# Optimization experiments

Measured on AMD Instinct MI355X. Metric: run time of the kernel, lower is better.

Reference implementation:

```python
import jax, jax.numpy as jnp
import numpy as np

EPS = 1e-5

def _conv(x, w, b):
    # NCHW x OIHW -> NCHW, stride 1, SAME padding (stencil center (1,1) of 3x3, or 1x1)
    y = jax.lax.conv_general_dilated(x, w, (1, 1), 'SAME',
                                     dimension_numbers=('NCHW', 'OIHW', 'NCHW'))
    return y + b[None, :, None, None]

def _bn(x, gamma, beta):
    # training-mode batchnorm: stats over (N, H, W) per channel
    mean = jnp.mean(x, axis=(0, 2, 3), keepdims=True)
    var = jnp.var(x, axis=(0, 2, 3), keepdims=True)
    xhat = (x - mean) * jax.lax.rsqrt(var + EPS)
    return xhat * gamma[None, :, None, None] + beta[None, :, None, None]

def setup_inputs() -> dict:
    key = jax.random.key(0)
    ks = jax.random.split(key, 12)
    B, Cin, Cout, H, W = 2, 64, 64, 512, 512
    s = 0.05
    return {
        'x':  jax.random.normal(ks[0], (B, Cin, H, W), jnp.float32),
        'w1': jax.random.normal(ks[1], (Cout, Cin, 3, 3), jnp.float32) * s,
        'b1': jnp.zeros((Cout,), jnp.float32),
        'g1': jnp.ones((Cout,), jnp.float32),
        'be1': jnp.zeros((Cout,), jnp.float32),
        'w2': jax.random.normal(ks[2], (Cout, Cout, 3, 3), jnp.float32) * s,
        'b2': jnp.zeros((Cout,), jnp.float32),
        'g2': jnp.ones((Cout,), jnp.float32),
        'be2': jnp.zeros((Cout,), jnp.float32),
        'wp': jax.random.normal(ks[3], (Cout, Cin, 1, 1), jnp.float32) * s,
        'bp': jnp.zeros((Cout,), jnp.float32),
        'gp': jnp.ones((Cout,), jnp.float32),
        'bep': jnp.zeros((Cout,), jnp.float32),
    }

def reference(x, w1, b1, g1, be1, w2, b2, g2, be2, wp, bp, gp, bep):
    # project branch: 1x1 conv ([(0,0)] stencil) + BN
    residual = _bn(_conv(x, wp, bp), gp, bep)
    # conv1: pad + 3x3 lattice conv (full cp stencil) + BN + Identity downsample + ReLU
    out = jax.nn.relu(_bn(_conv(x, w1, b1), g1, be1))
    # conv2: pad + 3x3 lattice conv + BN
    out = _bn(_conv(out, w2, b2), g2, be2)
    # residual add + output ReLU
    return jax.nn.relu(out + residual)
```

## Files before the change

kernel.cpp:

```cpp
#include <hip/hip_runtime.h>
#include <hip/hip_bf16.h>
#include <stdint.h>

typedef short short8 __attribute__((ext_vector_type(8)));
typedef float f32x4 __attribute__((ext_vector_type(4)));
typedef float f32x16 __attribute__((ext_vector_type(16)));
typedef unsigned int u32;
typedef unsigned short u16;

#define HH 512
#define WW 512
#define CC 64
#define PLANE (HH*WW)
#define NSTATF 524288.0f

#define KTW 32
#define HSTR 560
#define KBSTR 1120
#define SLOTB 4480
#define NSLOT 8
#define RINGB (NSLOT*SLOTB)
#define BOUNCEB 8192
#define NBC 1024
#define NBP 4096
#define K5S 260

__device__ __forceinline__ u16 f2bf(float f) {
  __hip_bfloat16 h = __float2bfloat16(f);
  return __builtin_bit_cast(u16, h);
}
__device__ __forceinline__ u32 pk2bf(float a, float b) {
  return (u32)f2bf(a) | ((u32)f2bf(b) << 16);
}
__device__ __forceinline__ float bf2f(u16 u) {
  u32 x = ((u32)u) << 16;
  return __builtin_bit_cast(float, x);
}
__device__ __forceinline__ void lds_barrier() {
  asm volatile("s_waitcnt lgkmcnt(0)" ::: "memory");
  __builtin_amdgcn_s_barrier();
  __builtin_amdgcn_sched_barrier(0);
}

__global__ __launch_bounds__(512) void kprep(const float* __restrict__ w1,
    const float* __restrict__ w2, const float* __restrict__ wp,
    u16* __restrict__ wb1, u16* __restrict__ wb2, u16* __restrict__ wbp)
{
  const int id = blockIdx.x*512 + threadIdx.x;
  const int lane = id & 63;
  if (id < 9216) {
    const float* w = (id < 4608) ? w1 : w2;
    u16* o = (id < 4608) ? wb1 : wb2;
    const int fid = (id < 4608) ? (id >> 6) : ((id - 4608) >> 6);
    const int ct4 = fid / 18, rem = fid % 18;
    const int tap = rem >> 1, kb = rem & 1;
    const int cout = ct4*16 + (lane & 15);
    const int k0c = kb*32 + (lane >> 4)*8;
    u32 ow[4];
#pragma unroll
    for (int p = 0; p < 4; ++p) {
      float a = w[(size_t)(cout*64 + k0c + p*2    )*9 + tap];
      float b = w[(size_t)(cout*64 + k0c + p*2 + 1)*9 + tap];
      ow[p] = pk2bf(a, b);
    }
    *(uint4*)(o + ((size_t)fid*64 + lane)*8) = make_uint4(ow[0],ow[1],ow[2],ow[3]);
  } else if (id < 9728) {
    const int fid = (id - 9216) >> 6;
    const int ct = fid >> 2, kb = fid & 3;
    const int cout = ct*32 + (lane & 31);
    const int cinb = kb*16 + (lane >> 5)*8;
    u32 ow[4];
#pragma unroll
    for (int p = 0; p < 4; ++p)
      ow[p] = pk2bf(wp[cout*64 + cinb + p*2], wp[cout*64 + cinb + p*2 + 1]);
    *(uint4*)(wbp + ((size_t)fid*64 + lane)*8) = make_uint4(ow[0],ow[1],ow[2],ow[3]);
  }
}

__global__ __launch_bounds__(256) void k0(const float* __restrict__ x,
    const u16* __restrict__ wbp,
    u16* __restrict__ xh, u16* __restrict__ yp,
    float* __restrict__ psp, float* __restrict__ pqp)
{
  __shared__ __align__(16) u32 Tp[32*260];
  __shared__ __align__(16) char B2[32768];
  const int tid = threadIdx.x;
  const int lane = tid & 63, wv = tid >> 6;
  const int ct = wv & 1, tg = wv >> 1;
  const int wt = blockIdx.x, h = blockIdx.y, n = blockIdx.z;
  const int w0 = wt*256;
  const int bid0 = (n*HH + h)*2 + wt;

  short8 wpf[4];
#pragma unroll
  for (int kb = 0; kb < 4; ++kb)
    wpf[kb] = *(const short8*)(wbp + ((size_t)(ct*4 + kb)*64 + lane)*8);

  const float* xp = x + (size_t)n*CC*PLANE + (size_t)h*WW + w0;
#pragma unroll
  for (int it = 0; it < 8; ++it) {
    const int j = it*256 + tid;
    const int c2 = j >> 6, w4 = (j & 63) << 2;
    const f32x4 a = *(const f32x4*)(xp + (size_t)(c2*2    )*PLANE + w4);
    const f32x4 b = *(const f32x4*)(xp + (size_t)(c2*2 + 1)*PLANE + w4);
    uint4 o;
    o.x = pk2bf(a[0], b[0]);
    o.y = pk2bf(a[1], b[1]);
    o.z = pk2bf(a[2], b[2]);
    o.w = pk2bf(a[3], b[3]);
    *(uint4*)(Tp + (u32)c2*260 + w4) = o;
  }
  __syncthreads();
  u16* op = xh + ((size_t)(n*HH + h)*WW + w0)*CC;
#pragma unroll
  for (int it = 0; it < 8; ++it) {
    const int j = it*256 + tid;
    const int w = j >> 3, c8 = j & 7;
    uint4 o;
    o.x = Tp[(u32)(c8*4 + 0)*260 + w];
    o.y = Tp[(u32)(c8*4 + 1)*260 + w];
    o.z = Tp[(u32)(c8*4 + 2)*260 + w];
    o.w = Tp[(u32)(c8*4 + 3)*260 + w];
    *(uint4*)(op + (size_t)w*CC + c8*8) = o;
    *(uint4*)(B2 + (((u32)(w*128 + c8*16)) ^ (((u32)(w & 7)) << 4))) = o;
  }
  __syncthreads();
  f32x16 pa[4];
  float s[16], q[16];
#pragma unroll
  for (int r = 0; r < 16; ++r) { s[r] = 0.f; q[r] = 0.f; }
#pragma unroll
  for (int ti = 0; ti < 4; ++ti) {
    const int tl = tg + ti*2;
    const int pos = tl*32 + (lane & 31);
    f32x16 acc;
#pragma unroll
    for (int r = 0; r < 16; ++r) acc[r] = 0.f;
#pragma unroll
    for (int kb = 0; kb < 4; ++kb) {
      const short8 bf = *(const short8*)(B2 +
          (((u32)(pos*128 + kb*32 + (lane>>5)*16)) ^ (((u32)(pos & 7)) << 4)));
      acc = __builtin_amdgcn_mfma_f32_32x32x16_bf16(wpf[kb], bf, acc, 0, 0, 0);
    }
#pragma unroll
    for (int r = 0; r < 16; ++r) {
      const float v = acc[r];
      pa[ti][r] = v; s[r] += v; q[r] = fmaf(v, v, q[r]);
    }
  }
  __syncthreads();
#pragma unroll
  for (int ti = 0; ti < 4; ++ti) {
    const int tl = tg + ti*2;
    const int pos = tl*32 + (lane & 31);
    const int rp[8] = {0,2,8,10,16,18,24,26};
#pragma unroll
    for (int p = 0; p < 8; ++p) {
      const int co = ct*32 + 4*(lane>>5) + rp[p];
      *(u32*)(B2 + (((u32)(pos*128 + co*2)) ^ (((u32)(pos & 7)) << 4))) =
          pk2bf(pa[ti][p*2], pa[ti][p*2+1]);
    }
  }
  __syncthreads();
  u16* opp = yp + ((size_t)(n*HH + h)*WW + w0)*CC;
#pragma unroll
  for (int it = 0; it < 8; ++it) {
    const int j = it*256 + tid;
    const int pos = j >> 3, qi = j & 7;
    const uint4 v = *(const uint4*)(B2 +
        (((u32)(pos*128 + qi*16)) ^ (((u32)(pos & 7)) << 4)));
    *(uint4*)((char*)opp + (size_t)pos*128 + qi*16) = v;
  }
#pragma unroll
  for (int d = 1; d <= 16; d <<= 1) {
#pragma unroll
    for (int r = 0; r < 16; ++r) {
      s[r] += __shfl_xor(s[r], d, 64);
      q[r] += __shfl_xor(q[r], d, 64);
    }
  }
  if ((lane & 31) == 0) {
#pragma unroll
    for (int r = 0; r < 16; ++r) {
      const int co = ct*32 + (r&3) + 8*(r>>2) + 4*(lane>>5);
      psp[(size_t)co*NBP + bid0*2 + tg] = s[r];
      pqp[(size_t)co*NBP + bid0*2 + tg] = q[r];
    }
  }
}

template<bool BNS>
__global__ __launch_bounds__(256, 2) void kconv(const u16* __restrict__ in,
    const u16* __restrict__ wb,
    const float* __restrict__ As, const float* __restrict__ Bs,
    u16* __restrict__ out, float* __restrict__ ps, float* __restrict__ pq)
{
  __shared__ __align__(16) char LB[RINGB + BOUNCEB + 512];
  float* sA = (float*)(LB + RINGB + BOUNCEB);
  float* sB = sA + 64;
  const int tid = threadIdx.x;
  const int lane = tid & 63, wv = tid >> 6;
  const int l15 = lane & 15, lq = lane >> 4;
  const int wt = blockIdx.x, hs = blockIdx.y, n = blockIdx.z;
  const int w0 = wt*KTW, h0 = hs*16;
  const int bid = (n*32 + hs)*16 + wt;

  if (BNS) {
    if (tid < 64) { sA[tid] = As[tid]; sB[tid] = Bs[tid]; }
    __syncthreads();
  }

  short8 wfr[18];
#pragma unroll
  for (int f = 0; f < 18; ++f)
    wfr[f] = *(const short8*)(wb + ((size_t)(wv*18 + f)*64 + lane)*8);

  float s4[4] = {0,0,0,0}, q4[4] = {0,0,0,0};
  const u16* inb = in + (size_t)n*PLANE*CC;
  const u32 co0 = (u32)((lq >> 1)*KBSTR + (lq & 1)*HSTR);
  const u32 co1 = co0 + 2*KBSTR;

  auto ld_one = [&](int j, int cl, int c8) -> uint4 {
    const int gh = h0 - 1 + j, gw = w0 - 1 + cl;
    if (((u32)gh < (u32)HH) && ((u32)gw < (u32)WW))
      return *(const uint4*)(inb + ((size_t)gh*WW + gw)*CC + c8*8);
    return make_uint4(0u,0u,0u,0u);
  };
  auto st_one = [&](int slot, int cl, int c8, uint4 v) {
    if (BNS) {
      const u32* uw = (const u32*)&v;
      u32 ow[4];
      const int cb = c8*8;
#pragma unroll
      for (int h2 = 0; h2 < 4; ++h2) {
        float f0 = fmaxf(bf2f((u16)(uw[h2] & 0xFFFFu)) * sA[cb+h2*2]   + sB[cb+h2*2],   0.f);
        float f1 = fmaxf(bf2f((u16)(uw[h2] >> 16))     * sA[cb+h2*2+1] + sB[cb+h2*2+1], 0.f);
        ow[h2] = pk2bf(f0, f1);
      }
      v = make_uint4(ow[0],ow[1],ow[2],ow[3]);
    }
    *(uint4*)(LB + (size_t)slot*SLOTB + (c8>>1)*KBSTR + (c8&1)*HSTR + cl*16) = v;
  };

  for (int idx = tid; idx < 4*272; idx += 256) {
    const int jj = idx / 272, rem = idx - jj*272;
    st_one(jj, rem >> 3, rem & 7, ld_one(jj, rem >> 3, rem & 7));
  }
  __syncthreads();

  uint4 st0, st1, st2;
  auto issue2 = [&](int jb) {
    { const int idx = tid;       const int jj = idx/272, rem = idx - jj*272;
      st0 = ld_one(jb + jj, rem >> 3, rem & 7); }
    { const int idx = 256 + tid; const int jj = idx/272, rem = idx - jj*272;
      st1 = ld_one(jb + jj, rem >> 3, rem & 7); }
    if (tid < 32) { const int idx = 512 + tid; const int jj = idx/272, rem = idx - jj*272;
      st2 = ld_one(jb + jj, rem >> 3, rem & 7); }
  };
  auto write2 = [&](int jb) {
    { const int idx = tid;       const int jj = idx/272, rem = idx - jj*272;
      st_one((jb + jj) & 7, rem >> 3, rem & 7, st0); }
    { const int idx = 256 + tid; const int jj = idx/272, rem = idx - jj*272;
      st_one((jb + jj) & 7, rem >> 3, rem & 7, st1); }
    if (tid < 32) { const int idx = 512 + tid; const int jj = idx/272, rem = idx - jj*272;
      st_one((jb + jj) & 7, rem >> 3, rem & 7, st2); }
  };

  issue2(4);

  for (int g = 0; g < 8; ++g) {
    if (g > 0) write2(2*g + 2);
    lds_barrier();
    if (g < 7) issue2(2*g + 4);

    const char* sb[4];
#pragma unroll
    for (int mi = 0; mi < 4; ++mi)
      sb[mi] = LB + (size_t)((2*g + mi) & 7)*SLOTB + l15*16;
    f32x4 a0t0, a0t1, a1t0, a1t1;
#pragma unroll
    for (int r = 0; r < 4; ++r) { a0t0[r]=0.f; a0t1[r]=0.f; a1t0[r]=0.f; a1t1[r]=0.f; }
#pragma unroll
    for (int t = 0; t < 2; ++t) {
      const int pb = t*16;
#pragma unroll
      for (int kb = 0; kb < 2; ++kb) {
        const u32 ck = kb ? co1 : co0;
#pragma unroll
        for (int mi = 0; mi < 4; ++mi) {
#pragma unroll
          for (int kw = 0; kw < 3; ++kw) {
            const short8 X = *(const short8*)(sb[mi] + ck + (u32)((pb + kw)*16));
            if (mi <= 2) {
              const short8 Wf = wfr[(mi*3 + kw)*2 + kb];
              if (t == 0) a0t0 = __builtin_amdgcn_mfma_f32_16x16x32_bf16(Wf, X, a0t0, 0,0,0);
              else        a0t1 = __builtin_amdgcn_mfma_f32_16x16x32_bf16(Wf, X, a0t1, 0,0,0);
            }
            if (mi >= 1) {
              const short8 Wf = wfr[((mi-1)*3 + kw)*2 + kb];
              if (t == 0) a1t0 = __builtin_amdgcn_mfma_f32_16x16x32_bf16(Wf, X, a1t0, 0,0,0);
              else        a1t1 = __builtin_amdgcn_mfma_f32_16x16x32_bf16(Wf, X, a1t1, 0,0,0);
            }
          }
        }
      }
    }
    {
      const int co = wv*16 + lq*4;
#pragma unroll
      for (int r = 0; r < 4; ++r) {
        s4[r] += a0t0[r] + a0t1[r] + a1t0[r] + a1t1[r];
        q4[r] = fmaf(a0t0[r], a0t0[r], q4[r]);
        q4[r] = fmaf(a0t1[r], a0t1[r], q4[r]);
        q4[r] = fmaf(a1t0[r], a1t0[r], q4[r]);
        q4[r] = fmaf(a1t1[r], a1t1[r], q4[r]);
      }
#pragma unroll
      for (int t = 0; t < 2; ++t) {
        const int pos = t*16 + l15;
        const u32 addr = ((u32)(pos*128 + co*2)) ^ (((u32)(pos & 7)) << 4);
        uint2 p0, p1;
        if (t == 0) {
          p0.x = pk2bf(a0t0[0], a0t0[1]); p0.y = pk2bf(a0t0[2], a0t0[3]);
          p1.x = pk2bf(a1t0[0], a1t0[1]); p1.y = pk2bf(a1t0[2], a1t0[3]);
        } else {
          p0.x = pk2bf(a0t1[0], a0t1[1]); p0.y = pk2bf(a0t1[2], a0t1[3]);
          p1.x = pk2bf(a1t1[0], a1t1[1]); p1.y = pk2bf(a1t1[2], a1t1[3]);
        }
        *(uint2*)(LB + RINGB + 0*4096 + addr) = p0;
        *(uint2*)(LB + RINGB + 1*4096 + addr) = p1;
      }
    }
    lds_barrier();
    {
      const int rowi = tid >> 7, tt = tid & 127;
      const int pos = tt >> 2, qb = (tt & 3)*32;
      const char* bb = LB + RINGB + rowi*4096;
      const u32 a0 = ((u32)(pos*128 + qb)) ^ (((u32)(pos & 7)) << 4);
      const uint4 v0 = *(const uint4*)(bb + a0);
      const uint4 v1 = *(const uint4*)(bb + (a0 ^ 16u));
      char* dst = (char*)out + ((size_t)((n*HH + h0 + 2*g + rowi)*WW + w0 + pos))*128 + qb;
      *(uint4*)dst = v0;
      *(uint4*)(dst + 16) = v1;
    }
  }

#pragma unroll
  for (int d = 1; d <= 8; d <<= 1) {
#pragma unroll
    for (int r = 0; r < 4; ++r) {
      s4[r] += __shfl_xor(s4[r], d, 64);
      q4[r] += __shfl_xor(q4[r], d, 64);
    }
  }
  if (l15 == 0) {
#pragma unroll
    for (int r = 0; r < 4; ++r) {
      const int co = wv*16 + lq*4 + r;
      ps[(size_t)co*NBC + bid] = s4[r];
      pq[(size_t)co*NBC + bid] = q4[r];
    }
  }
}

__global__ __launch_bounds__(256) void kfin2(
    const float* __restrict__ psA, const float* __restrict__ pqA,
    const float* __restrict__ gA, const float* __restrict__ beA,
    float* __restrict__ AA, float* __restrict__ BA, int cntA,
    const float* __restrict__ psB, const float* __restrict__ pqB,
    const float* __restrict__ gB, const float* __restrict__ beB,
    float* __restrict__ AB, float* __restrict__ BB, int cntB)
{
  const int blk = blockIdx.x;
  const bool second = blk >= 64;
  const int c = blk & 63;
  const float* psx = second ? psB : psA;
  const float* pqx = second ? pqB : pqA;
  const float* g  = second ? gB  : gA;
  const float* be = second ? beB : beA;
  float* A  = second ? AB : AA;
  float* Bc = second ? BB : BA;
  const int cnt = second ? cntB : cntA;

  const int t = threadIdx.x;
  float sv = 0.f, s2 = 0.f;
  const float* pr = psx + (size_t)c*cnt;
  const float* qr = pqx + (size_t)c*cnt;
  for (int k = t; k < cnt; k += 256) { sv += pr[k]; s2 += qr[k]; }
#pragma unroll
  for (int d = 1; d < 64; d <<= 1) { sv += __shfl_xor(sv, d, 64); s2 += __shfl_xor(s2, d, 64); }
  __shared__ float as_[4], aq_[4];
  if ((t & 63) == 0) { as_[t >> 6] = sv; aq_[t >> 6] = s2; }
  __syncthreads();
  if (t == 0) {
    sv = as_[0] + as_[1] + as_[2] + as_[3];
    s2 = aq_[0] + aq_[1] + aq_[2] + aq_[3];
    const float mean = sv / NSTATF;
    const float var = s2 / NSTATF - mean*mean;
    const float istd = rsqrtf(var + 1e-5f);
    const float a = g[c] * istd;
    A[c] = a;
    Bc[c] = be[c] - mean * a;
  }
}

__global__ __launch_bounds__(256) void k5(const u16* __restrict__ y2, const u16* __restrict__ yp,
    const float* __restrict__ A2, const float* __restrict__ B2c,
    const float* __restrict__ Ap, const float* __restrict__ Bp,
    float* __restrict__ outp)
{
  __shared__ float T[CC*K5S];
  __shared__ float cA2[64], cB2[64], cAp[64], cBp[64];
  const int tid = threadIdx.x;
  const int lane = tid & 63, wv = tid >> 6;
  const int wt = blockIdx.x, h = blockIdx.y, n = blockIdx.z;
  const int w0 = wt*256;
  if (tid < 64) { cA2[tid] = A2[tid]; cB2[tid] = B2c[tid]; cAp[tid] = Ap[tid]; cBp[tid] = Bp[tid]; }
  __syncthreads();
  const u16* p2 = y2 + ((size_t)(n*HH + h)*WW + w0)*CC;
  const u16* pp = yp + ((size_t)(n*HH + h)*WW + w0)*CC;
#pragma unroll
  for (int it = 0; it < 8; ++it) {
    const int j = it*256 + tid;
    const int w = j >> 3, c8 = j & 7;
    const uint4 u2 = *(const uint4*)(p2 + (size_t)w*CC + c8*8);
    const uint4 up = *(const uint4*)(pp + (size_t)w*CC + c8*8);
    const u32* m2 = (const u32*)&u2;
    const u32* mp = (const u32*)&up;
    const u32 sw = ((u32)(c8 & 3)) << 3;
#pragma unroll
    for (int h2 = 0; h2 < 4; ++h2) {
      const int c = c8*8 + h2*2;
      const float a = bf2f((u16)(m2[h2] & 0xFFFFu)), b = bf2f((u16)(m2[h2] >> 16));
      const float ra = bf2f((u16)(mp[h2] & 0xFFFFu)), rb = bf2f((u16)(mp[h2] >> 16));
      const u32 wsw = (u32)w ^ sw;
      T[(u32)(c    )*K5S + wsw] = fmaxf(a*cA2[c]   + cB2[c]   + ra*cAp[c]   + cBp[c],   0.f);
      T[(u32)(c + 1)*K5S + wsw] = fmaxf(b*cA2[c+1] + cB2[c+1] + rb*cAp[c+1] + cBp[c+1], 0.f);
    }
  }
  __syncthreads();
#pragma unroll
  for (int cc = 0; cc < 16; ++cc) {
    const int c = cc*4 + wv;
    const u32 sw = ((u32)((c >> 3) & 3)) << 3;
    const u32 idx = (u32)c*K5S + (((u32)lane*4) ^ sw);
    const f32x4 v = *(const f32x4*)(T + idx);
    *(f32x4*)(outp + ((size_t)((n*CC + c)*HH + h))*WW + w0 + lane*4) = v;
  }
}

extern "C" void kernel_launch(void* const* d_in, const int* in_sizes, int n_in,
                              void* d_out, int out_size, void* d_ws, size_t ws_size,
                              hipStream_t stream)
{
  (void)in_sizes; (void)n_in; (void)out_size;
  const float* x   = (const float*)d_in[0];
  const float* w1  = (const float*)d_in[1];
  const float* g1  = (const float*)d_in[3];
  const float* be1 = (const float*)d_in[4];
  const float* w2  = (const float*)d_in[5];
  const float* g2  = (const float*)d_in[7];
  const float* be2 = (const float*)d_in[8];
  const float* wp  = (const float*)d_in[9];
  const float* gp  = (const float*)d_in[11];
  const float* bep = (const float*)d_in[12];

  const size_t TENB = (size_t)2*CC*PLANE*2;
  char* ws = (char*)d_ws;
  u16* bufA = (u16*)ws;
  u16* bufB = (u16*)(ws + TENB);
  u16* bufC = (u16*)(ws + TENB*2);
  char* aux = ws + TENB*3;
  u16* wb1 = (u16*)aux;
  u16* wb2 = (u16*)(aux + 73728);
  u16* wbp = (u16*)(aux + 147456);
  float* ps1 = (float*)(aux + 155648);
  float* pq1 = ps1 + 64*NBC;
  float* ps2 = pq1 + 64*NBC;
  float* pq2 = ps2 + 64*NBC;
  float* psp = pq2 + 64*NBC;
  float* pqp = psp + 64*NBP;
  float* A1  = pqp + 64*NBP;
  float* B1  = A1 + 64;
  float* A2  = B1 + 64;
  float* B2c = A2 + 64;
  float* Ap  = B2c + 64;
  float* Bp  = Ap + 64;
  const size_t need = (size_t)(Bp + 64 - (float*)ws) * 4;
  if (ws_size < need) return;

  kprep<<<19, 512, 0, stream>>>(w1, w2, wp, wb1, wb2, wbp);
  k0<<<dim3(2, HH, 2), 256, 0, stream>>>(x, wbp, bufA, bufC, psp, pqp);
  kconv<false><<<dim3(16, 32, 2), 256, 0, stream>>>(bufA, wb1, nullptr, nullptr,
                                                    bufB, ps1, pq1);
  kfin2<<<128, 256, 0, stream>>>(ps1, pq1, g1, be1, A1, B1, NBC,
                                 psp, pqp, gp, bep, Ap, Bp, NBP);
  kconv<true><<<dim3(16, 32, 2), 256, 0, stream>>>(bufB, wb2, A1, B1,
                                                   bufA, ps2, pq2);
  kfin2<<<64, 256, 0, stream>>>(ps2, pq2, g2, be2, A2, B2c, NBC,
                                ps2, pq2, g2, be2, A2, B2c, NBC);
  k5<<<dim3(2, HH, 2), 256, 0, stream>>>(bufA, bufC, A2, B2c, Ap, Bp, (float*)d_out);
}
```

Baseline: 229.6 us.

## Fuse 1x1 projection conv into first 3x3 conv kernel, swizzle k0 transpose

```diff
diff --git a/kernel.cpp b/kernel.cpp
--- a/kernel.cpp
+++ b/kernel.cpp
@@ -4,7 +4,6 @@
 
 typedef short short8 __attribute__((ext_vector_type(8)));
 typedef float f32x4 __attribute__((ext_vector_type(4)));
-typedef float f32x16 __attribute__((ext_vector_type(16)));
 typedef unsigned int u32;
 typedef unsigned short u16;
 
@@ -20,9 +19,8 @@
 #define SLOTB 4480
 #define NSLOT 8
 #define RINGB (NSLOT*SLOTB)
-#define BOUNCEB 8192
+#define BOUNCEB 16384
 #define NBC 1024
-#define NBP 4096
 #define K5S 260
 
 __device__ __forceinline__ u16 f2bf(float f) {
@@ -66,36 +64,23 @@
     *(uint4*)(o + ((size_t)fid*64 + lane)*8) = make_uint4(ow[0],ow[1],ow[2],ow[3]);
   } else if (id < 9728) {
     const int fid = (id - 9216) >> 6;
-    const int ct = fid >> 2, kb = fid & 3;
-    const int cout = ct*32 + (lane & 31);
-    const int cinb = kb*16 + (lane >> 5)*8;
+    const int ct4 = fid >> 1, kb = fid & 1;
+    const int cout = ct4*16 + (lane & 15);
+    const int k0c = kb*32 + (lane >> 4)*8;
     u32 ow[4];
 #pragma unroll
     for (int p = 0; p < 4; ++p)
-      ow[p] = pk2bf(wp[cout*64 + cinb + p*2], wp[cout*64 + cinb + p*2 + 1]);
+      ow[p] = pk2bf(wp[cout*64 + k0c + p*2], wp[cout*64 + k0c + p*2 + 1]);
     *(uint4*)(wbp + ((size_t)fid*64 + lane)*8) = make_uint4(ow[0],ow[1],ow[2],ow[3]);
   }
 }
 
-__global__ __launch_bounds__(256) void k0(const float* __restrict__ x,
-    const u16* __restrict__ wbp,
-    u16* __restrict__ xh, u16* __restrict__ yp,
-    float* __restrict__ psp, float* __restrict__ pqp)
+__global__ __launch_bounds__(256) void k0(const float* __restrict__ x, u16* __restrict__ xh)
 {
   __shared__ __align__(16) u32 Tp[32*260];
-  __shared__ __align__(16) char B2[32768];
   const int tid = threadIdx.x;
-  const int lane = tid & 63, wv = tid >> 6;
-  const int ct = wv & 1, tg = wv >> 1;
   const int wt = blockIdx.x, h = blockIdx.y, n = blockIdx.z;
   const int w0 = wt*256;
-  const int bid0 = (n*HH + h)*2 + wt;
-
-  short8 wpf[4];
-#pragma unroll
-  for (int kb = 0; kb < 4; ++kb)
-    wpf[kb] = *(const short8*)(wbp + ((size_t)(ct*4 + kb)*64 + lane)*8);
-
   const float* xp = x + (size_t)n*CC*PLANE + (size_t)h*WW + w0;
 #pragma unroll
   for (int it = 0; it < 8; ++it) {
@@ -108,7 +93,7 @@
     o.y = pk2bf(a[1], b[1]);
     o.z = pk2bf(a[2], b[2]);
     o.w = pk2bf(a[3], b[3]);
-    *(uint4*)(Tp + (u32)c2*260 + w4) = o;
+    *(uint4*)(Tp + (u32)c2*260 + (u32)(w4 ^ (4*(c2 >> 2)))) = o;
   }
   __syncthreads();
   u16* op = xh + ((size_t)(n*HH + h)*WW + w0)*CC;
@@ -116,84 +101,23 @@
   for (int it = 0; it < 8; ++it) {
     const int j = it*256 + tid;
     const int w = j >> 3, c8 = j & 7;
+    const u32 wsw = (u32)(w ^ (4*c8));
     uint4 o;
-    o.x = Tp[(u32)(c8*4 + 0)*260 + w];
-    o.y = Tp[(u32)(c8*4 + 1)*260 + w];
-    o.z = Tp[(u32)(c8*4 + 2)*260 + w];
-    o.w = Tp[(u32)(c8*4 + 3)*260 + w];
+    o.x = Tp[(u32)(c8*4 + 0)*260 + wsw];
+    o.y = Tp[(u32)(c8*4 + 1)*260 + wsw];
+    o.z = Tp[(u32)(c8*4 + 2)*260 + wsw];
+    o.w = Tp[(u32)(c8*4 + 3)*260 + wsw];
     *(uint4*)(op + (size_t)w*CC + c8*8) = o;
-    *(uint4*)(B2 + (((u32)(w*128 + c8*16)) ^ (((u32)(w & 7)) << 4))) = o;
-  }
-  __syncthreads();
-  f32x16 pa[4];
-  float s[16], q[16];
-#pragma unroll
-  for (int r = 0; r < 16; ++r) { s[r] = 0.f; q[r] = 0.f; }
-#pragma unroll
-  for (int ti = 0; ti < 4; ++ti) {
-    const int tl = tg + ti*2;
-    const int pos = tl*32 + (lane & 31);
-    f32x16 acc;
-#pragma unroll
-    for (int r = 0; r < 16; ++r) acc[r] = 0.f;
-#pragma unroll
-    for (int kb = 0; kb < 4; ++kb) {
-      const short8 bf = *(const short8*)(B2 +
-          (((u32)(pos*128 + kb*32 + (lane>>5)*16)) ^ (((u32)(pos & 7)) << 4)));
-      acc = __builtin_amdgcn_mfma_f32_32x32x16_bf16(wpf[kb], bf, acc, 0, 0, 0);
-    }
-#pragma unroll
-    for (int r = 0; r < 16; ++r) {
-      const float v = acc[r];
-      pa[ti][r] = v; s[r] += v; q[r] = fmaf(v, v, q[r]);
-    }
-  }
-  __syncthreads();
-#pragma unroll
-  for (int ti = 0; ti < 4; ++ti) {
-    const int tl = tg + ti*2;
-    const int pos = tl*32 + (lane & 31);
-    const int rp[8] = {0,2,8,10,16,18,24,26};
-#pragma unroll
-    for (int p = 0; p < 8; ++p) {
-      const int co = ct*32 + 4*(lane>>5) + rp[p];
-      *(u32*)(B2 + (((u32)(pos*128 + co*2)) ^ (((u32)(pos & 7)) << 4))) =
-          pk2bf(pa[ti][p*2], pa[ti][p*2+1]);
-    }
-  }
-  __syncthreads();
-  u16* opp = yp + ((size_t)(n*HH + h)*WW + w0)*CC;
-#pragma unroll
-  for (int it = 0; it < 8; ++it) {
-    const int j = it*256 + tid;
-    const int pos = j >> 3, qi = j & 7;
-    const uint4 v = *(const uint4*)(B2 +
-        (((u32)(pos*128 + qi*16)) ^ (((u32)(pos & 7)) << 4)));
-    *(uint4*)((char*)opp + (size_t)pos*128 + qi*16) = v;
-  }
-#pragma unroll
-  for (int d = 1; d <= 16; d <<= 1) {
-#pragma unroll
-    for (int r = 0; r < 16; ++r) {
-      s[r] += __shfl_xor(s[r], d, 64);
-      q[r] += __shfl_xor(q[r], d, 64);
-    }
-  }
-  if ((lane & 31) == 0) {
-#pragma unroll
-    for (int r = 0; r < 16; ++r) {
-      const int co = ct*32 + (r&3) + 8*(r>>2) + 4*(lane>>5);
-      psp[(size_t)co*NBP + bid0*2 + tg] = s[r];
-      pqp[(size_t)co*NBP + bid0*2 + tg] = q[r];
-    }
-  }
-}
-
-template<bool BNS>
+  }
+}
+
+template<bool BNS, bool PROJ>
 __global__ __launch_bounds__(256, 2) void kconv(const u16* __restrict__ in,
-    const u16* __restrict__ wb,
+    const u16* __restrict__ wb, const u16* __restrict__ wbp,
     const float* __restrict__ As, const float* __restrict__ Bs,
-    u16* __restrict__ out, float* __restrict__ ps, float* __restrict__ pq)
+    u16* __restrict__ out, u16* __restrict__ yp,
+    float* __restrict__ ps, float* __restrict__ pq,
+    float* __restrict__ psp, float* __restrict__ pqp)
 {
   __shared__ __align__(16) char LB[RINGB + BOUNCEB + 512];
   float* sA = (float*)(LB + RINGB + BOUNCEB);
@@ -214,8 +138,15 @@
 #pragma unroll
   for (int f = 0; f < 18; ++f)
     wfr[f] = *(const short8*)(wb + ((size_t)(wv*18 + f)*64 + lane)*8);
+  short8 wpf[2];
+  if constexpr (PROJ) {
+#pragma unroll
+    for (int kb = 0; kb < 2; ++kb)
+      wpf[kb] = *(const short8*)(wbp + ((size_t)(wv*2 + kb)*64 + lane)*8);
+  }
 
   float s4[4] = {0,0,0,0}, q4[4] = {0,0,0,0};
+  float sp4[4] = {0,0,0,0}, qp4[4] = {0,0,0,0};
   const u16* inb = in + (size_t)n*PLANE*CC;
   const u32 co0 = (u32)((lq >> 1)*KBSTR + (lq & 1)*HSTR);
   const u32 co1 = co0 + 2*KBSTR;
@@ -278,8 +209,12 @@
     for (int mi = 0; mi < 4; ++mi)
       sb[mi] = LB + (size_t)((2*g + mi) & 7)*SLOTB + l15*16;
     f32x4 a0t0, a0t1, a1t0, a1t1;
-#pragma unroll
-    for (int r = 0; r < 4; ++r) { a0t0[r]=0.f; a0t1[r]=0.f; a1t0[r]=0.f; a1t1[r]=0.f; }
+    f32x4 p0t0, p0t1, p1t0, p1t1;
+#pragma unroll
+    for (int r = 0; r < 4; ++r) {
+      a0t0[r]=0.f; a0t1[r]=0.f; a1t0[r]=0.f; a1t1[r]=0.f;
+      p0t0[r]=0.f; p0t1[r]=0.f; p1t0[r]=0.f; p1t1[r]=0.f;
+    }
 #pragma unroll
     for (int t = 0; t < 2; ++t) {
       const int pb = t*16;
@@ -301,6 +236,16 @@
               if (t == 0) a1t0 = __builtin_amdgcn_mfma_f32_16x16x32_bf16(Wf, X, a1t0, 0,0,0);
               else        a1t1 = __builtin_amdgcn_mfma_f32_16x16x32_bf16(Wf, X, a1t1, 0,0,0);
             }
+            if constexpr (PROJ) {
+              if (kw == 1 && mi == 1) {
+                if (t == 0) p0t0 = __builtin_amdgcn_mfma_f32_16x16x32_bf16(wpf[kb], X, p0t0, 0,0,0);
+                else        p0t1 = __builtin_amdgcn_mfma_f32_16x16x32_bf16(wpf[kb], X, p0t1, 0,0,0);
+              }
+              if (kw == 1 && mi == 2) {
+                if (t == 0) p1t0 = __builtin_amdgcn_mfma_f32_16x16x32_bf16(wpf[kb], X, p1t0, 0,0,0);
+                else        p1t1 = __builtin_amdgcn_mfma_f32_16x16x32_bf16(wpf[kb], X, p1t1, 0,0,0);
+              }
+            }
           }
         }
       }
@@ -315,24 +260,59 @@
         q4[r] = fmaf(a1t0[r], a1t0[r], q4[r]);
         q4[r] = fmaf(a1t1[r], a1t1[r], q4[r]);
       }
+      if constexpr (PROJ) {
+#pragma unroll
+        for (int r = 0; r < 4; ++r) {
+          sp4[r] += p0t0[r] + p0t1[r] + p1t0[r] + p1t1[r];
+          qp4[r] = fmaf(p0t0[r], p0t0[r], qp4[r]);
+          qp4[r] = fmaf(p0t1[r], p0t1[r], qp4[r]);
+          qp4[r] = fmaf(p1t0[r], p1t0[r], qp4[r]);
+          qp4[r] = fmaf(p1t1[r], p1t1[r], qp4[r]);
+        }
+      }
 #pragma unroll
       for (int t = 0; t < 2; ++t) {
         const int pos = t*16 + l15;
         const u32 addr = ((u32)(pos*128 + co*2)) ^ (((u32)(pos & 7)) << 4);
-        uint2 p0, p1;
+        uint2 c0, c1;
         if (t == 0) {
-          p0.x = pk2bf(a0t0[0], a0t0[1]); p0.y = pk2bf(a0t0[2], a0t0[3]);
-          p1.x = pk2bf(a1t0[0], a1t0[1]); p1.y = pk2bf(a1t0[2], a1t0[3]);
+          c0.x = pk2bf(a0t0[0], a0t0[1]); c0.y = pk2bf(a0t0[2], a0t0[3]);
+          c1.x = pk2bf(a1t0[0], a1t0[1]); c1.y = pk2bf(a1t0[2], a1t0[3]);
         } else {
-          p0.x = pk2bf(a0t1[0], a0t1[1]); p0.y = pk2bf(a0t1[2], a0t1[3]);
-          p1.x = pk2bf(a1t1[0], a1t1[1]); p1.y = pk2bf(a1t1[2], a1t1[3]);
+          c0.x = pk2bf(a0t1[0], a0t1[1]); c0.y = pk2bf(a0t1[2], a0t1[3]);
+          c1.x = pk2bf(a1t1[0], a1t1[1]); c1.y = pk2bf(a1t1[2], a1t1[3]);
         }
-        *(uint2*)(LB + RINGB + 0*4096 + addr) = p0;
-        *(uint2*)(LB + RINGB + 1*4096 + addr) = p1;
+        *(uint2*)(LB + RINGB + 0*4096 + addr) = c0;
+        *(uint2*)(LB + RINGB + 1*4096 + addr) = c1;
+        if constexpr (PROJ) {
+          uint2 d0, d1;
+          if (t == 0) {
+            d0.x = pk2bf(p0t0[0], p0t0[1]); d0.y = pk2bf(p0t0[2], p0t0[3]);
+            d1.x = pk2bf(p1t0[0], p1t0[1]); d1.y = pk2bf(p1t0[2], p1t0[3]);
+          } else {
+            d0.x = pk2bf(p0t1[0], p0t1[1]); d0.y = pk2bf(p0t1[2], p0t1[3]);
+            d1.x = pk2bf(p1t1[0], p1t1[1]); d1.y = pk2bf(p1t1[2], p1t1[3]);
+          }
+          *(uint2*)(LB + RINGB + 2*4096 + addr) = d0;
+          *(uint2*)(LB + RINGB + 3*4096 + addr) = d1;
+        }
       }
     }
     lds_barrier();
-    {
+    if constexpr (PROJ) {
+      const int rowi = tid >> 6, tt = tid & 63;
+      const int pos = tt >> 1, half = (tt & 1)*64;
+      const char* bb = LB + RINGB + rowi*4096;
+      u16* base = (rowi < 2) ? out : yp;
+      const int orow = h0 + 2*g + (rowi & 1);
+      char* dst = (char*)base + ((size_t)((n*HH + orow)*WW + w0 + pos))*128 + half;
+      const u32 sw = ((u32)(pos & 7)) << 4;
+#pragma unroll
+      for (int k2 = 0; k2 < 4; ++k2) {
+        const uint4 v = *(const uint4*)(bb + (((u32)(pos*128 + half + k2*16)) ^ sw));
+        *(uint4*)(dst + k2*16) = v;
+      }
+    } else {
       const int rowi = tid >> 7, tt = tid & 127;
       const int pos = tt >> 2, qb = (tt & 3)*32;
       const char* bb = LB + RINGB + rowi*4096;
@@ -359,6 +339,24 @@
       const int co = wv*16 + lq*4 + r;
       ps[(size_t)co*NBC + bid] = s4[r];
       pq[(size_t)co*NBC + bid] = q4[r];
+    }
+  }
+  if constexpr (PROJ) {
+#pragma unroll
+    for (int d = 1; d <= 8; d <<= 1) {
+#pragma unroll
+      for (int r = 0; r < 4; ++r) {
+        sp4[r] += __shfl_xor(sp4[r], d, 64);
+        qp4[r] += __shfl_xor(qp4[r], d, 64);
+      }
+    }
+    if (l15 == 0) {
+#pragma unroll
+      for (int r = 0; r < 4; ++r) {
+        const int co = wv*16 + lq*4 + r;
+        psp[(size_t)co*NBC + bid] = sp4[r];
+        pqp[(size_t)co*NBC + bid] = qp4[r];
+      }
     }
   }
 }
@@ -479,8 +477,8 @@
   float* ps2 = pq1 + 64*NBC;
   float* pq2 = ps2 + 64*NBC;
   float* psp = pq2 + 64*NBC;
-  float* pqp = psp + 64*NBP;
-  float* A1  = pqp + 64*NBP;
+  float* pqp = psp + 64*NBC;
+  float* A1  = pqp + 64*NBC;
   float* B1  = A1 + 64;
   float* A2  = B1 + 64;
   float* B2c = A2 + 64;
@@ -490,13 +488,13 @@
   if (ws_size < need) return;
 
   kprep<<<19, 512, 0, stream>>>(w1, w2, wp, wb1, wb2, wbp);
-  k0<<<dim3(2, HH, 2), 256, 0, stream>>>(x, wbp, bufA, bufC, psp, pqp);
-  kconv<false><<<dim3(16, 32, 2), 256, 0, stream>>>(bufA, wb1, nullptr, nullptr,
-                                                    bufB, ps1, pq1);
+  k0<<<dim3(2, HH, 2), 256, 0, stream>>>(x, bufA);
+  kconv<false, true><<<dim3(16, 32, 2), 256, 0, stream>>>(bufA, wb1, wbp, nullptr, nullptr,
+                                                          bufB, bufC, ps1, pq1, psp, pqp);
   kfin2<<<128, 256, 0, stream>>>(ps1, pq1, g1, be1, A1, B1, NBC,
-                                 psp, pqp, gp, bep, Ap, Bp, NBP);
-  kconv<true><<<dim3(16, 32, 2), 256, 0, stream>>>(bufB, wb2, A1, B1,
-                                                   bufA, ps2, pq2);
+                                 psp, pqp, gp, bep, Ap, Bp, NBC);
+  kconv<true, false><<<dim3(16, 32, 2), 256, 0, stream>>>(bufB, wb2, nullptr, A1, B1,
+                                                          bufA, nullptr, ps2, pq2, nullptr, nullptr);
   kfin2<<<64, 256, 0, stream>>>(ps2, pq2, g2, be2, A2, B2c, NBC,
                                 ps2, pq2, g2, be2, A2, B2c, NBC);
   k5<<<dim3(2, HH, 2), 256, 0, stream>>>(bufA, bufC, A2, B2c, Ap, Bp, (float*)d_out);
```

Result: faster. 223.5 us (-2.7%).
